# Kernel optimization log

Hardware: AMD Instinct MI355X
Metric: run time of the kernel (lower is better)

The kernel has to match this reference:

```python
import jax, jax.numpy as jnp
import numpy as np

B, N, HID = 2, 2048, 1024
H, DH = 16, 64

def apply_rope(x, rope):
    # x: [B,H,N,D], rope: [B,N,D] interpreted as interleaved (cos, sin) pairs
    Bx, Hx, Nx, D = x.shape
    xp = x.reshape(Bx, Hx, Nx, D // 2, 2)
    rp = rope.reshape(Bx, 1, Nx, D // 2, 2)
    cos, sin = rp[..., 0], rp[..., 1]
    x0, x1 = xp[..., 0], xp[..., 1]
    out = jnp.stack([x0 * cos - x1 * sin, x1 * cos + x0 * sin], axis=-1)
    return out.reshape(Bx, Hx, Nx, D)


def setup_inputs() -> dict:
    key = jax.random.key(0)
    k1, k2, k3, k4 = jax.random.split(key, 4)
    x = jax.random.normal(k1, (B, N, HID), dtype=jnp.float32)
    rope = jax.random.normal(k2, (B, N, DH), dtype=jnp.float32)
    Wqkv = jax.random.normal(k3, (3 * H * DH, HID), dtype=jnp.float32) * (HID ** -0.5)
    Wout = jax.random.normal(k4, (HID, H * DH), dtype=jnp.float32) * ((H * DH) ** -0.5)
    return {"x": x, "rope": rope, "Wqkv": Wqkv, "Wout": Wout}


def reference(x, rope, Wqkv, Wout):
    scale = DH ** -0.5
    qkv = jnp.einsum('bnd,ed->bne', x, Wqkv)          # [B,N,3*H*DH]
    qkv = qkv.reshape(B, N, 3, H, DH)
    qkv = jnp.transpose(qkv, (2, 0, 3, 1, 4))          # [3,B,H,N,DH]
    q, k, v = qkv[0], qkv[1], qkv[2]
    q = apply_rope(q, rope)
    k = apply_rope(k, rope)
    attn = jnp.einsum('bhnd,bhmd->bhnm', q, k) * scale  # [B,H,N,N]
    attn = jax.nn.softmax(attn, axis=-1)
    out = jnp.einsum('bhnm,bhmd->bhnd', attn, v)        # [B,H,N,DH]
    out = jnp.transpose(out, (0, 2, 1, 3)).reshape(B, N, H * DH)
    return jnp.einsum('bne,de->bnd', out, Wout)
```

## Files before the change

### kernel.cpp

```cpp
#include <hip/hip_runtime.h>
#include <stdint.h>
#include <stddef.h>

typedef __bf16 bf16;
typedef __bf16 bf16x2 __attribute__((ext_vector_type(2)));
typedef __bf16 bf16x4 __attribute__((ext_vector_type(4)));
typedef __bf16 bf16x8 __attribute__((ext_vector_type(8)));
typedef float f32x2 __attribute__((ext_vector_type(2)));
typedef float f32x4 __attribute__((ext_vector_type(4)));
typedef float f32x16 __attribute__((ext_vector_type(16)));

constexpr int Bb = 2, Nn = 2048, HID = 1024, Hh = 16, DH = 64;
constexpr int MTOK = Bb * Nn;
constexpr int E3 = 3 * Hh * DH;

__global__ void cast3_kernel(const float* __restrict__ x, const float* __restrict__ wqkv,
                             const float* __restrict__ wout,
                             bf16* __restrict__ xb, bf16* __restrict__ wqkvb,
                             bf16* __restrict__ woutb) {
  constexpr int N1 = MTOK * HID / 4;
  constexpr int N2 = N1 + E3 * HID / 4;
  int i = blockIdx.x * 256 + threadIdx.x;
  const float* src;
  bf16* dst;
  int off;
  if (i < N1)      { src = x;    dst = xb;    off = i; }
  else if (i < N2) { src = wqkv; dst = wqkvb; off = i - N1; }
  else             { src = wout; dst = woutb; off = i - N2; }
  f32x4 v = reinterpret_cast<const f32x4*>(src)[off];
  bf16x4 o;
#pragma unroll
  for (int j = 0; j < 4; ++j) o[j] = (bf16)v[j];
  reinterpret_cast<bf16x4*>(dst)[off] = o;
}

template <bool OUT_BF16>
__global__ __launch_bounds__(256) void gemm_bt(const bf16* __restrict__ A,
                                               const bf16* __restrict__ Bt,
                                               void* __restrict__ Cp,
                                               int M, int N, int K) {
  __shared__ __align__(16) bf16 As[2][128 * 32];
  __shared__ __align__(16) bf16 Bs[2][128 * 32];
  const int tid = threadIdx.x;
  const int lane = tid & 63;
  const int wave = tid >> 6;
  const int wr = wave >> 1, wc = wave & 1;
  const int bm = blockIdx.x, bn = blockIdx.y;
  const int frow = lane & 15;
  const int fk = (lane >> 4) * 8;
  const int c0 = wave * 128 + lane;

  f32x4 acc[4][4] = {};

  for (int k0 = 0; k0 < K; k0 += 64) {
#pragma unroll
    for (int hk = 0; hk < 2; ++hk)
#pragma unroll
      for (int i = 0; i < 2; ++i) {
        int c = c0 + i * 64;
        int row = c >> 2;
        int col = (c & 3) * 8;
        const bf16* ga = A + (size_t)(bm * 128 + row) * K + k0 + hk * 32 + col;
        const bf16* gb = Bt + (size_t)(bn * 128 + row) * K + k0 + hk * 32 + col;
        __builtin_amdgcn_global_load_lds((const __attribute__((address_space(1))) void*)ga,
                                         (__attribute__((address_space(3))) void*)(As[hk] + c * 8),
                                         16, 0, 0);
        __builtin_amdgcn_global_load_lds((const __attribute__((address_space(1))) void*)gb,
                                         (__attribute__((address_space(3))) void*)(Bs[hk] + c * 8),
                                         16, 0, 0);
      }
    __syncthreads();
#pragma unroll
    for (int hk = 0; hk < 2; ++hk) {
      bf16x8 af[4], bfr[4];
#pragma unroll
      for (int m = 0; m < 4; ++m)
        af[m] = *reinterpret_cast<const bf16x8*>(As[hk] + (wr * 64 + m * 16 + frow) * 32 + fk);
#pragma unroll
      for (int n = 0; n < 4; ++n)
        bfr[n] = *reinterpret_cast<const bf16x8*>(Bs[hk] + (wc * 64 + n * 16 + frow) * 32 + fk);
#pragma unroll
      for (int m = 0; m < 4; ++m)
#pragma unroll
        for (int n = 0; n < 4; ++n)
          acc[m][n] = __builtin_amdgcn_mfma_f32_16x16x32_bf16(af[m], bfr[n], acc[m][n], 0, 0, 0);
    }
    __syncthreads();
  }

  const int r0 = bm * 128 + wr * 64;
  const int cc0 = bn * 128 + wc * 64;
#pragma unroll
  for (int m = 0; m < 4; ++m)
#pragma unroll
    for (int n = 0; n < 4; ++n)
#pragma unroll
      for (int r = 0; r < 4; ++r) {
        int row = r0 + m * 16 + (lane >> 4) * 4 + r;
        int col = cc0 + n * 16 + frow;
        if (OUT_BF16)
          ((bf16*)Cp)[(size_t)row * N + col] = (bf16)acc[m][n][r];
        else
          ((float*)Cp)[(size_t)row * N + col] = acc[m][n][r];
      }
}

__device__ __forceinline__ int kappa(int a) {
  return (((a >> 2) ^ (a >> 3)) & 1) ? (a ^ 12) : a;
}

__global__ __launch_bounds__(256) void rope_pack(const bf16* __restrict__ qkvb,
                                                 const float* __restrict__ rope,
                                                 bf16* __restrict__ qpk,
                                                 bf16* __restrict__ kpk,
                                                 bf16* __restrict__ vpk) {
  __shared__ bf16 qs[128][66];
  __shared__ bf16 ks[128][66];
  __shared__ bf16 vs[128][66];
  const int bh = blockIdx.y;
  const int b = bh >> 4;
  const int h = bh & 15;
  const int n0 = blockIdx.x * 128;
  const int t = threadIdx.x;

  constexpr float QS = 0.125f * 1.44269504088896340736f;

  for (int it = 0; it < 16; ++it) {
    int p = it * 256 + t;
    int nl = p >> 5, i = p & 31;
    int n = n0 + nl;
    size_t rowbase = (size_t)(b * Nn + n);
    const bf16* src = qkvb + rowbase * E3 + h * DH + 2 * i;
    f32x2 cs = *reinterpret_cast<const f32x2*>(rope + rowbase * DH + 2 * i);
    float c = cs[0], sn = cs[1];
    bf16x2 qv = *reinterpret_cast<const bf16x2*>(src);
    bf16x2 kv = *reinterpret_cast<const bf16x2*>(src + HID);
    bf16x2 vv = *reinterpret_cast<const bf16x2*>(src + 2 * HID);
    float q0 = (float)qv[0], q1 = (float)qv[1];
    float k0 = (float)kv[0], k1 = (float)kv[1];
    qs[nl][2 * i]     = (bf16)((q0 * c - q1 * sn) * QS);
    qs[nl][2 * i + 1] = (bf16)((q1 * c + q0 * sn) * QS);
    ks[nl][2 * i]     = (bf16)(k0 * c - k1 * sn);
    ks[nl][2 * i + 1] = (bf16)(k1 * c + k0 * sn);
    vs[nl][2 * i]     = vv[0];
    vs[nl][2 * i + 1] = vv[1];
  }
  __syncthreads();

  const int lane2 = t & 63;
  const int dd = t >> 6;
  const int lo2 = lane2 & 31, hi2 = lane2 >> 5;
  const int lok = kappa(lo2);
#pragma unroll
  for (int kbq = 0; kbq < 4; ++kbq) {
    int col = dd * 16 + hi2 * 8;
    bf16x8 q8 = *reinterpret_cast<const bf16x8*>(&qs[kbq * 32 + lo2][col]);
    bf16x8 k8 = *reinterpret_cast<const bf16x8*>(&ks[kbq * 32 + lok][col]);
    size_t base = ((((size_t)bh * 64 + (n0 >> 5) + kbq) * 4 + dd) * 64 + lane2) * 8;
    *reinterpret_cast<bf16x8*>(qpk + base) = q8;
    *reinterpret_cast<bf16x8*>(kpk + base) = k8;
  }

#pragma unroll
  for (int wi = 0; wi < 4; ++wi) {
    int id = wi * 256 + t;
    int lane3 = id & 63;
    int sub = id >> 6;
    int kt = sub >> 3, dt = (sub >> 2) & 1, kbi = sub & 3;
    int lo3 = lane3 & 31, hi3 = lane3 >> 5;
    bf16x8 v8;
#pragma unroll
    for (int j = 0; j < 8; ++j)
      v8[j] = vs[kt * 64 + kbi * 16 + hi3 * 8 + j][dt * 32 + lo3];
    size_t vbase = ((((size_t)bh * 32 + (n0 >> 6) + kt) * 8 + dt * 4 + kbi) * 64 + lane3) * 8;
    *reinterpret_cast<bf16x8*>(vpk + vbase) = v8;
  }
}

__global__ __launch_bounds__(512, 4) void attn_kernel(const bf16* __restrict__ qpk,
                                                      const bf16* __restrict__ kpk,
                                                      const bf16* __restrict__ vpk,
                                                      bf16* __restrict__ outb) {
  __shared__ __align__(16) char kvlds[2][2][16384];
  const int tid = threadIdx.x;
  const int lane = tid & 63;
  const int wave = tid >> 6;
  const int grp = wave >> 2;
  const int wg = wave & 3;
  const int bid = blockIdx.x;
  const int xcd = bid & 7;
  const int idx = bid >> 3;
  const int bh = xcd * 4 + (idx >> 4);
  const int qt = idx & 15;
  const int b = bh >> 4, h = bh & 15;
  const int lo = lane & 31;
  const int hi = lane >> 5;
  const int q0 = qt * 128 + wg * 32;

  bf16x8 qf[4];
#pragma unroll
  for (int d = 0; d < 4; ++d)
    qf[d] = *reinterpret_cast<const bf16x8*>(
        qpk + ((((size_t)bh * 64 + qt * 4 + wg) * 4 + d) * 64 + lane) * 8);

  f32x16 o0 = {}, o1 = {};
  float lacc[16];
#pragma unroll
  for (int r = 0; r < 16; ++r) lacc[r] = 0.f;

  auto cvtpk = [](float a, float b) {
    unsigned w;
    asm("v_cvt_pk_bf16_f32 %0, %1, %2" : "=v"(w) : "v"(a), "v"(b));
    return w;
  };

  const bf16* kg = kpk + (size_t)bh * 131072 + wg * 512 + lane * 8;
  const bf16* vg = vpk + (size_t)bh * 131072 + wg * 512 + lane * 8;

  auto stage = [&](int til, int buf) {
    char* ld = &kvlds[grp][buf][wg * 1024];
    const bf16* kk = kg + (size_t)(grp * 16 + til) * 4096;
    const bf16* vv = vg + (size_t)(grp * 16 + til) * 4096;
#pragma unroll
    for (int i = 0; i < 2; ++i) {
      __builtin_amdgcn_global_load_lds((const __attribute__((address_space(1))) void*)(kk + i * 2048),
                                       (__attribute__((address_space(3))) void*)(ld + i * 4096),
                                       16, 0, 0);
      __builtin_amdgcn_global_load_lds((const __attribute__((address_space(1))) void*)(vv + i * 2048),
                                       (__attribute__((address_space(3))) void*)(ld + 8192 + i * 4096),
                                       16, 0, 0);
    }
  };

  auto substep = [&](int cur) {
    const char* base = &kvlds[grp][cur][lane * 16];
    bf16x8 kf[8], vf[8];
#pragma unroll
    for (int c = 0; c < 8; ++c) {
      kf[c] = *reinterpret_cast<const bf16x8*>(base + c * 1024);
      vf[c] = *reinterpret_cast<const bf16x8*>(base + 8192 + c * 1024);
    }

    f32x16 s0 = {}, s1 = {};
#pragma unroll
    for (int d = 0; d < 4; ++d) {
      s0 = __builtin_amdgcn_mfma_f32_32x32x16_bf16(kf[d], qf[d], s0, 0, 0, 0);
      s1 = __builtin_amdgcn_mfma_f32_32x32x16_bf16(kf[4 + d], qf[d], s1, 0, 0, 0);
    }

    float e[32];
#pragma unroll
    for (int r = 0; r < 16; ++r) e[r] = __builtin_amdgcn_exp2f(s0[r]);
#pragma unroll
    for (int r = 0; r < 16; ++r) e[16 + r] = __builtin_amdgcn_exp2f(s1[r]);

#pragma unroll
    for (int r = 0; r < 16; ++r) lacc[r] += e[r] + e[16 + r];

    union { unsigned w[4]; bf16x8 v8; } pb[4];
#pragma unroll
    for (int c = 0; c < 4; ++c)
#pragma unroll
      for (int w = 0; w < 4; ++w)
        pb[c].w[w] = cvtpk(e[c * 8 + 2 * w], e[c * 8 + 2 * w + 1]);

#pragma unroll
    for (int kbi = 0; kbi < 4; ++kbi) {
      o0 = __builtin_amdgcn_mfma_f32_32x32x16_bf16(vf[kbi], pb[kbi].v8, o0, 0, 0, 0);
      o1 = __builtin_amdgcn_mfma_f32_32x32x16_bf16(vf[4 + kbi], pb[kbi].v8, o1, 0, 0, 0);
    }
  };

  stage(0, 0);
  __syncthreads();

  for (int t = 0; t < 16; ++t) {
    const int cur = t & 1;
    if (t < 15) stage(t + 1, cur ^ 1);
    substep(cur);
    __syncthreads();
  }

  float lrun;
  {
    float u[8];
#pragma unroll
    for (int r = 0; r < 8; ++r) u[r] = lacc[r] + lacc[r + 8];
#pragma unroll
    for (int r = 0; r < 4; ++r) u[r] += u[r + 4];
    lrun = (u[0] + u[2]) + (u[1] + u[3]);
    lrun += __shfl_xor(lrun, 32);
  }

  float* scr = (float*)&kvlds[0][0][0];
  if (grp == 1) {
#pragma unroll
    for (int r = 0; r < 16; ++r) scr[r * 256 + wg * 64 + lane] = o0[r];
#pragma unroll
    for (int r = 0; r < 16; ++r) scr[(16 + r) * 256 + wg * 64 + lane] = o1[r];
    scr[8192 + wg * 64 + lane] = lrun;
  }
  __syncthreads();
  if (grp == 0) {
    float l1 = scr[8192 + wg * 64 + lane];
    float invl = 1.0f / (lrun + l1);
#pragma unroll
    for (int dt = 0; dt < 2; ++dt) {
#pragma unroll
      for (int g = 0; g < 4; ++g) {
        bf16x4 ov;
#pragma unroll
        for (int j = 0; j < 4; ++j) {
          int r = g * 4 + j;
          float mine = dt ? o1[r] : o0[r];
          float partner = scr[(dt * 16 + r) * 256 + wg * 64 + lane];
          ov[j] = (bf16)((mine + partner) * invl);
        }
        int dh = dt * 32 + g * 8 + hi * 4;
        *reinterpret_cast<bf16x4*>(outb + (size_t)(b * Nn + q0 + lo) * HID + h * DH + dh) = ov;
      }
    }
  }
}

extern "C" void kernel_launch(void* const* d_in, const int* in_sizes, int n_in,
                              void* d_out, int out_size, void* d_ws, size_t ws_size,
                              hipStream_t stream) {
  const float* x = (const float*)d_in[0];
  const float* rope = (const float*)d_in[1];
  const float* Wqkv = (const float*)d_in[2];
  const float* Wout = (const float*)d_in[3];
  float* out = (float*)d_out;

  char* w = (char*)d_ws;
  size_t off = 0;
  auto alloc = [&](size_t bytes) -> void* {
    void* p = w + off;
    off += (bytes + 255) & ~(size_t)255;
    return p;
  };
  bf16* xb    = (bf16*)alloc((size_t)MTOK * HID * 2);
  bf16* wqkvb = (bf16*)alloc((size_t)E3 * HID * 2);
  bf16* woutb = (bf16*)alloc((size_t)HID * HID * 2);
  bf16* qkvb  = (bf16*)alloc((size_t)MTOK * E3 * 2);
  bf16* qpk   = (bf16*)alloc((size_t)Bb * Hh * Nn * DH * 2);
  bf16* kpk   = (bf16*)alloc((size_t)Bb * Hh * Nn * DH * 2);
  bf16* vpk   = (bf16*)alloc((size_t)Bb * Hh * Nn * DH * 2);
  bf16* attno = (bf16*)alloc((size_t)MTOK * HID * 2);

  constexpr int CAST4 = (MTOK * HID + E3 * HID + HID * HID) / 4;
  cast3_kernel<<<CAST4 / 256, 256, 0, stream>>>(x, Wqkv, Wout, xb, wqkvb, woutb);

  gemm_bt<true><<<dim3(MTOK / 128, E3 / 128), 256, 0, stream>>>(xb, wqkvb, qkvb, MTOK, E3, HID);

  rope_pack<<<dim3(Nn / 128, Bb * Hh), 256, 0, stream>>>(qkvb, rope, qpk, kpk, vpk);

  attn_kernel<<<dim3(512), 512, 0, stream>>>(qpk, kpk, vpk, attno);

  gemm_bt<false><<<dim3(MTOK / 128, HID / 128), 256, 0, stream>>>(attno, woutb, out, MTOK, HID, HID);
}
```

Measured before the change: 117.8 us.

## Pipeline GEMM K-loop with prefetch and reorder attention V/K LDS reads

The GEMM K-loop is restructured to prefetch the next 32-wide K slice into the alternate LDS buffer while MFMAs consume the current one, with one barrier per step instead of two per 64-wide step. This aims to overlap global-to-LDS loads with compute. In the attention substep, the V fragments are now read from LDS before the K fragments, and an empty asm statement pins them. This changes how the LDS reads are scheduled around the QK MFMAs. The prefetch relies on a single barrier per iteration with a double buffer. That risks a race if the async LDS loads of step h+1 can land before other waves finish reading buffer (h+1)&1 from step h-1.

New measurement: 118.7 us. No clear change (+0.7%).

```diff
diff --git a/kernel.cpp b/kernel.cpp
--- a/kernel.cpp
+++ b/kernel.cpp
@@ -52,39 +52,45 @@
 
   f32x4 acc[4][4] = {};
 
-  for (int k0 = 0; k0 < K; k0 += 64) {
-#pragma unroll
-    for (int hk = 0; hk < 2; ++hk)
-#pragma unroll
-      for (int i = 0; i < 2; ++i) {
-        int c = c0 + i * 64;
-        int row = c >> 2;
-        int col = (c & 3) * 8;
-        const bf16* ga = A + (size_t)(bm * 128 + row) * K + k0 + hk * 32 + col;
-        const bf16* gb = Bt + (size_t)(bn * 128 + row) * K + k0 + hk * 32 + col;
-        __builtin_amdgcn_global_load_lds((const __attribute__((address_space(1))) void*)ga,
-                                         (__attribute__((address_space(3))) void*)(As[hk] + c * 8),
-                                         16, 0, 0);
-        __builtin_amdgcn_global_load_lds((const __attribute__((address_space(1))) void*)gb,
-                                         (__attribute__((address_space(3))) void*)(Bs[hk] + c * 8),
-                                         16, 0, 0);
-      }
-    __syncthreads();
-#pragma unroll
-    for (int hk = 0; hk < 2; ++hk) {
-      bf16x8 af[4], bfr[4];
-#pragma unroll
-      for (int m = 0; m < 4; ++m)
-        af[m] = *reinterpret_cast<const bf16x8*>(As[hk] + (wr * 64 + m * 16 + frow) * 32 + fk);
+  const int nh = K >> 5;
+
+  auto stageh = [&](int h) {
+    const int buf = h & 1;
+    const int kcol = h * 32;
+#pragma unroll
+    for (int i = 0; i < 2; ++i) {
+      int c = c0 + i * 64;
+      int row = c >> 2;
+      int col = (c & 3) * 8;
+      const bf16* ga = A + (size_t)(bm * 128 + row) * K + kcol + col;
+      const bf16* gb = Bt + (size_t)(bn * 128 + row) * K + kcol + col;
+      __builtin_amdgcn_global_load_lds((const __attribute__((address_space(1))) void*)ga,
+                                       (__attribute__((address_space(3))) void*)(As[buf] + c * 8),
+                                       16, 0, 0);
+      __builtin_amdgcn_global_load_lds((const __attribute__((address_space(1))) void*)gb,
+                                       (__attribute__((address_space(3))) void*)(Bs[buf] + c * 8),
+                                       16, 0, 0);
+    }
+  };
+
+  stageh(0);
+  __syncthreads();
+
+  for (int h = 0; h < nh; ++h) {
+    if (h + 1 < nh) stageh(h + 1);
+    const int buf = h & 1;
+    bf16x8 af[4], bfr[4];
+#pragma unroll
+    for (int m = 0; m < 4; ++m)
+      af[m] = *reinterpret_cast<const bf16x8*>(As[buf] + (wr * 64 + m * 16 + frow) * 32 + fk);
+#pragma unroll
+    for (int n = 0; n < 4; ++n)
+      bfr[n] = *reinterpret_cast<const bf16x8*>(Bs[buf] + (wc * 64 + n * 16 + frow) * 32 + fk);
+#pragma unroll
+    for (int m = 0; m < 4; ++m)
 #pragma unroll
       for (int n = 0; n < 4; ++n)
-        bfr[n] = *reinterpret_cast<const bf16x8*>(Bs[hk] + (wc * 64 + n * 16 + frow) * 32 + fk);
-#pragma unroll
-      for (int m = 0; m < 4; ++m)
-#pragma unroll
-        for (int n = 0; n < 4; ++n)
-          acc[m][n] = __builtin_amdgcn_mfma_f32_16x16x32_bf16(af[m], bfr[n], acc[m][n], 0, 0, 0);
-    }
+        acc[m][n] = __builtin_amdgcn_mfma_f32_16x16x32_bf16(af[m], bfr[n], acc[m][n], 0, 0, 0);
     __syncthreads();
   }
 
@@ -234,12 +240,18 @@
 
   auto substep = [&](int cur) {
     const char* base = &kvlds[grp][cur][lane * 16];
-    bf16x8 kf[8], vf[8];
-#pragma unroll
-    for (int c = 0; c < 8; ++c) {
+    bf16x8 vf[8];
+#pragma unroll
+    for (int c = 0; c < 8; ++c)
+      vf[c] = *reinterpret_cast<const bf16x8*>(base + 8192 + c * 1024);
+#pragma unroll
+    for (int c = 0; c < 8; ++c)
+      asm volatile("" :: "v"(vf[c]));
+
+    bf16x8 kf[8];
+#pragma unroll
+    for (int c = 0; c < 8; ++c)
       kf[c] = *reinterpret_cast<const bf16x8*>(base + c * 1024);
-      vf[c] = *reinterpret_cast<const bf16x8*>(base + 8192 + c * 1024);
-    }
 
     f32x16 s0 = {}, s1 = {};
 #pragma unroll
```
